# Kernel tuning notes

Measured on AMD Instinct MI355X. Metric: run time of the kernel, lower is better.

The kernel has to match this reference:

```python
import jax, jax.numpy as jnp
import numpy as np

P = 128; D = 128; A = 128
NS = D * A            # sinogram nodes
NP = P * P            # pixel nodes
N = NS + NP           # total graph nodes
EPS = 1e-5
_PNAMES = ["af_w1","af_b1","af_p1","af_bn_g","af_bn_b","af_w2","af_b2","af_p2","af_w3","af_b3","af_p3","af_w4","af_b4","af_p4","af_w5","af_b5","af_p5","gcn_w","gcn_b","sr_w1","sr_b1","sr_p1","sr_w2","sr_b2","sr_p2","sr_w3","sr_b3","sr_p3"]


def _conv(x, w, b, pad):
    y = jax.lax.conv_general_dilated(x, w, (1, 1), [(pad, pad), (pad, pad)],
                                     dimension_numbers=("NCHW", "OIHW", "NCHW"))
    return y + b[None, :, None, None]


def _prelu(x, a):
    return jnp.where(x >= 0, x, a * x)


def _bn(x, g, b):
    # BatchNorm2d in training mode: biased batch stats over (N,H,W)
    m = x.mean(axis=(0, 2, 3), keepdims=True)
    v = x.var(axis=(0, 2, 3), keepdims=True)
    return (x - m) * jax.lax.rsqrt(v + EPS) * g[None, :, None, None] + b[None, :, None, None]


def _forward(sino, edge_index, edge_weight, p):
    # AndrewCNN sinogram filter: 1 -> 64 -> 64 -> 64 -> 64 -> 8, 7x7 convs
    h = _prelu(_conv(sino, p["af_w1"], p["af_b1"], 3), p["af_p1"])
    h = _bn(h, p["af_bn_g"], p["af_bn_b"])
    h = _prelu(_conv(h, p["af_w2"], p["af_b2"], 3), p["af_p2"])
    h = _prelu(_conv(h, p["af_w3"], p["af_b3"], 3), p["af_p3"])
    h = _prelu(_conv(h, p["af_w4"], p["af_b4"], 3), p["af_p4"])
    h = _prelu(_conv(h, p["af_w5"], p["af_b5"], 3), p["af_p5"])   # [B,8,D,A]
    B, F = h.shape[0], h.shape[1]
    # build_nodes_features (source_to_target): sino nodes first, zero pixel nodes
    flat_sino = h.transpose(0, 2, 3, 1).reshape(B, NS, F)
    x = jnp.concatenate([flat_sino, jnp.zeros((B, NP, F), h.dtype)], axis=1)  # [B,N,8]
    # GCNConv(8,10): lin -> gcn_norm with self loops -> scatter-add at targets -> +bias
    xl = x @ p["gcn_w"]                                            # [B,N,10]
    row, col = edge_index[0], edge_index[1]
    loop = jnp.arange(N)
    row2 = jnp.concatenate([row, loop])
    col2 = jnp.concatenate([col, loop])
    w2 = jnp.concatenate([edge_weight, jnp.ones((N,), edge_weight.dtype)])
    deg = jnp.zeros((N,), xl.dtype).at[col2].add(w2)
    dis = jnp.where(deg > 0, jax.lax.rsqrt(jnp.maximum(deg, EPS * 0 + 1e-30)), 0.0)
    norm = dis[row2] * w2 * dis[col2]                              # [E+N]
    msgs = xl[:, row2, :] * norm[None, :, None]                    # [B,E+N,10]
    agg = jnp.zeros_like(xl).at[:, col2, :].add(msgs) + p["gcn_b"]
    # keep pixel nodes, reshape to image grid
    img = agg[:, NS:, :].transpose(0, 2, 1).reshape(B, -1, P, P)   # [B,10,P,P]
    # SRNET: 10 -> 64 (9x9) -> 32 (1x1) -> 1 (5x5)
    o = _prelu(_conv(img, p["sr_w1"], p["sr_b1"], 4), p["sr_p1"])
    o = _prelu(_conv(o,   p["sr_w2"], p["sr_b2"], 0), p["sr_p2"])
    o = _prelu(_conv(o,   p["sr_w3"], p["sr_b3"], 2), p["sr_p3"])
    return o


def setup_inputs() -> dict:
    f = jnp.float32
    ks = jax.random.split(jax.random.key(0), 16)
    B, E = 4, 2097152
    def rn(k, shape, s):
        return jax.random.normal(k, shape, f) * s
    inp = {
        "sino": jax.random.normal(ks[0], (B, 1, D, A), f),
        "edge_index": jax.random.randint(ks[1], (2, E), 0, N),
        "edge_weight": jax.random.uniform(ks[2], (E,), f),
    }
    kw = jax.random.split(ks[3], 9)
    inp["af_w1"] = rn(kw[0], (64, 1, 7, 7), 0.2)
    inp["af_w2"] = rn(kw[1], (64, 64, 7, 7), 0.03)
    inp["af_w3"] = rn(kw[2], (64, 64, 7, 7), 0.03)
    inp["af_w4"] = rn(kw[3], (64, 64, 7, 7), 0.03)
    inp["af_w5"] = rn(kw[4], (8, 64, 7, 7), 0.03)
    inp["gcn_w"] = rn(kw[5], (8, 10), 0.3)
    inp["sr_w1"] = rn(kw[6], (64, 10, 9, 9), 0.05)
    inp["sr_w2"] = rn(kw[7], (32, 64, 1, 1), 0.18)
    inp["sr_w3"] = rn(kw[8], (1, 32, 5, 5), 0.05)
    for nm, c in [("af_b1", 64), ("af_b2", 64), ("af_b3", 64), ("af_b4", 64), ("af_b5", 8), ("sr_b1", 64), ("sr_b2", 32), ("sr_b3", 1)]:
        inp[nm] = jnp.zeros((c,), f)
    inp["gcn_b"] = jnp.zeros((10,), f)
    inp["af_bn_g"] = jnp.ones((64,), f)
    inp["af_bn_b"] = jnp.zeros((64,), f)
    for nm in ["af_p1", "af_p2", "af_p3", "af_p4", "af_p5", "sr_p1", "sr_p2", "sr_p3"]:
        inp[nm] = jnp.array(0.25, f)
    return inp


def reference(sino, edge_index, edge_weight, af_w1, af_b1, af_p1, af_bn_g, af_bn_b, af_w2, af_b2, af_p2, af_w3, af_b3, af_p3, af_w4, af_b4, af_p4, af_w5, af_b5, af_p5, gcn_w, gcn_b, sr_w1, sr_b1, sr_p1, sr_w2, sr_b2, sr_p2, sr_w3, sr_b3, sr_p3):
    p = dict(zip(_PNAMES, (af_w1, af_b1, af_p1, af_bn_g, af_bn_b, af_w2, af_b2, af_p2, af_w3, af_b3, af_p3, af_w4, af_b4, af_p4, af_w5, af_b5, af_p5, gcn_w, gcn_b, sr_w1, sr_b1, sr_p1, sr_w2, sr_b2, sr_p2, sr_w3, sr_b3, sr_p3)))
    return _forward(sino, edge_index, edge_weight, p)
```

## Files before the change

kernel.cpp:

```cpp
#include <hip/hip_runtime.h>

static constexpr int NS = 16384;

typedef __attribute__((ext_vector_type(8))) short bf16x8;
typedef __attribute__((ext_vector_type(4))) float f32x4;

__device__ inline unsigned short bf16_rne(float x) {
  unsigned u = __float_as_uint(x);
  unsigned r = u + 0x7FFF + ((u >> 16) & 1);
  return (unsigned short)(r >> 16);
}

__global__ void k_wtrans(const float* __restrict__ w, float* __restrict__ wT,
                         int CO, int CI_IN, int CI_OUT, int KS) {
  int i = blockIdx.x * 256 + threadIdx.x;
  int tot = KS * KS * CI_OUT * CO;
  if (i >= tot) return;
  int co = i % CO;
  int r = i / CO;
  int ci = r % CI_OUT;
  int t = r / CI_OUT;
  int ky = t / KS, kx = t % KS;
  float v = 0.f;
  if (ci < CI_IN) v = w[((co * CI_IN + ci) * KS + ky) * KS + kx];
  wT[i] = v;
}

__global__ void k_wpack(const float* __restrict__ w, unsigned short* __restrict__ wpk) {
  int i = blockIdx.x * 256 + threadIdx.x;
  if (i >= 49 * 64 * 64) return;
  int co = i & 63, r = i >> 6;
  int ci = r & 63, tap = r >> 6;
  float v = w[(co * 64 + ci) * 49 + tap];
  unsigned short hi = bf16_rne(v);
  float hif = __uint_as_float((unsigned)hi << 16);
  unsigned short lo = bf16_rne(v - hif);
  int ks = ci >> 5, k32 = ci & 31;
  int lane = ((k32 >> 3) << 4) | (co & 15);
  int j = ci & 7, nt = co >> 4;
  size_t base = ((size_t)(((tap * 2 + ks) * 4 + nt) * 2) * 64 + lane) * 8 + j;
  wpk[base] = hi;
  wpk[base + 512] = lo;
}

__global__ void k_wpack5(const float* __restrict__ w5,
                         unsigned short* __restrict__ wpk) {
  int i = blockIdx.x * 256 + threadIdx.x;
  if (i >= 196 * 512) return;
  int j = i & 7, l = (i >> 3) & 63, f = i >> 9;
  int sp = f & 1, r = f >> 1;
  int ks = r & 1, tap = r >> 1;
  int co = l & 15;
  int k32 = ((l >> 4) << 3) + j;
  int ci = ks * 32 + k32;
  float v = (co < 8) ? w5[(co * 64 + ci) * 49 + tap] : 0.f;
  unsigned short hi = bf16_rne(v);
  unsigned short outv;
  if (sp == 0) {
    outv = hi;
  } else {
    float hif = __uint_as_float((unsigned)hi << 16);
    outv = bf16_rne(v - hif);
  }
  wpk[i] = outv;
}

__global__ void k_wpacks(const float* __restrict__ sw1,
                         unsigned short* __restrict__ wpk) {
  int i = blockIdx.x * 256 + threadIdx.x;
  if (i >= 360 * 512) return;
  int j = i & 7, l = (i >> 3) & 63, f = i >> 9;
  int sp = f & 1, nt = (f >> 1) & 3;
  int r3 = f >> 3, p = r3 % 5, ky = r3 / 5;
  int co = nt * 16 + (l & 15);
  int k = ((l >> 4) << 3) + j;
  int kx = 2 * p + (k >> 4);
  int ci = k & 15;
  float v = (ci < 10 && kx < 9) ? sw1[((co * 10 + ci) * 9 + ky) * 9 + kx] : 0.f;
  unsigned short hi = bf16_rne(v);
  unsigned short outv;
  if (sp == 0) {
    outv = hi;
  } else {
    float hif = __uint_as_float((unsigned)hi << 16);
    outv = bf16_rne(v - hif);
  }
  wpk[i] = outv;
}

__global__ __launch_bounds__(128) void k_conv1(
    const float* __restrict__ sino, const float* __restrict__ wT1,
    const float* __restrict__ b1, const float* __restrict__ p1,
    float* __restrict__ out) {
  int b = blockIdx.x >> 7, y = blockIdx.x & 127, x = threadIdx.x;
  float acc[64];
#pragma unroll
  for (int i = 0; i < 64; ++i) acc[i] = 0.f;
#pragma unroll
  for (int ky = 0; ky < 7; ++ky) {
    int yy = y + ky - 3;
#pragma unroll
    for (int kx = 0; kx < 7; ++kx) {
      int xx = x + kx - 3;
      float v = (yy >= 0 && yy < 128 && xx >= 0 && xx < 128)
                    ? sino[(b * 128 + yy) * 128 + xx]
                    : 0.f;
      const float* wr = wT1 + (ky * 7 + kx) * 64;
#pragma unroll
      for (int co = 0; co < 64; ++co) acc[co] += v * wr[co];
    }
  }
  float a = p1[0];
  float* op = out + ((size_t)(b * 134 + y + 3) * 134 + x + 3) * 64;
#pragma unroll
  for (int co = 0; co < 64; ++co) {
    float v = acc[co] + b1[co];
    op[co] = v >= 0.f ? v : a * v;
  }
}

__global__ __launch_bounds__(256) void k_bnstats(const float* __restrict__ x1p,
                                                 double* __restrict__ bnsum) {
  int c = threadIdx.x & 63, sl = threadIdx.x >> 6;
  double s = 0.0, q = 0.0;
  int base = blockIdx.x * 512 + sl * 128;
  for (int i = 0; i < 128; ++i) {
    int p = base + i;
    int b = p >> 14, y = (p >> 7) & 127, x = p & 127;
    double v = (double)x1p[((size_t)(b * 134 + y + 3) * 134 + x + 3) * 64 + c];
    s += v;
    q += v * v;
  }
  __shared__ double red[2][4][64];
  red[0][sl][c] = s;
  red[1][sl][c] = q;
  __syncthreads();
  if (sl == 0) {
    s = red[0][0][c] + red[0][1][c] + red[0][2][c] + red[0][3][c];
    q = red[1][0][c] + red[1][1][c] + red[1][2][c] + red[1][3][c];
    atomicAdd(&bnsum[c], s);
    atomicAdd(&bnsum[64 + c], q);
  }
}

__global__ void k_bnfinal(const double* __restrict__ bnsum, float* __restrict__ bnsc,
                          const float* __restrict__ g, const float* __restrict__ bb) {
  int c = threadIdx.x;
  if (c >= 64) return;
  double m = bnsum[c] * (1.0 / 65536.0);
  double v = bnsum[64 + c] * (1.0 / 65536.0) - m * m;
  double sc = (double)g[c] * rsqrt(v + 1e-5);
  bnsc[c] = (float)sc;
  bnsc[64 + c] = (float)((double)bb[c] - m * sc);
}

__global__ __launch_bounds__(256) void k_bnapply(
    const float* __restrict__ x1p, const float* __restrict__ bnsc,
    unsigned short* __restrict__ oh, unsigned short* __restrict__ ol) {
  int i = blockIdx.x * 256 + threadIdx.x;
  if (i >= 4 * 128 * 128 * 16) return;
  int g = i & 15, p = i >> 4;
  int b = p >> 14, y = (p >> 7) & 127, x = p & 127;
  size_t base = ((size_t)(b * 134 + y + 3) * 134 + x + 3) * 64 + g * 4;
  float4 v = *(const float4*)(x1p + base);
  int c = g * 4;
  v.x = v.x * bnsc[c + 0] + bnsc[64 + c + 0];
  v.y = v.y * bnsc[c + 1] + bnsc[64 + c + 1];
  v.z = v.z * bnsc[c + 2] + bnsc[64 + c + 2];
  v.w = v.w * bnsc[c + 3] + bnsc[64 + c + 3];
  unsigned short h0 = bf16_rne(v.x), h1 = bf16_rne(v.y);
  unsigned short h2 = bf16_rne(v.z), h3 = bf16_rne(v.w);
  unsigned short l0 = bf16_rne(v.x - __uint_as_float((unsigned)h0 << 16));
  unsigned short l1 = bf16_rne(v.y - __uint_as_float((unsigned)h1 << 16));
  unsigned short l2 = bf16_rne(v.z - __uint_as_float((unsigned)h2 << 16));
  unsigned short l3 = bf16_rne(v.w - __uint_as_float((unsigned)h3 << 16));
  *(ushort4*)(oh + base) = make_ushort4(h0, h1, h2, h3);
  *(ushort4*)(ol + base) = make_ushort4(l0, l1, l2, l3);
}

__global__ __launch_bounds__(256) void k_convm(
    const unsigned short* __restrict__ inh, const unsigned short* __restrict__ inl,
    const unsigned short* __restrict__ wpk, const float* __restrict__ bias,
    const float* __restrict__ alpha, unsigned short* __restrict__ outh,
    unsigned short* __restrict__ outl) {
  int i0 = (int)((blockIdx.x & 7) * 64 + (blockIdx.x >> 3));
  int b = i0 >> 7, y = i0 & 127;
  int tid = threadIdx.x, l = tid & 63;
  int wv = tid >> 6;
  int pxb = (wv & 1) * 64;
  int coh = wv >> 1;
  int lg = l >> 4, lm = l & 15;

  __shared__ unsigned short hbuf[2][134 * 44];
  __shared__ unsigned short lbuf[2][134 * 44];

  f32x4 acc[4][2];
#pragma unroll
  for (int mt = 0; mt < 4; ++mt)
#pragma unroll
    for (int ntl = 0; ntl < 2; ++ntl) acc[mt][ntl] = (f32x4){0.f, 0.f, 0.f, 0.f};

  for (int ch = 0; ch < 64; ch += 32) {
    auto stage = [&](int ky, int s) {
      const unsigned short* gh = inh + ((size_t)(b * 134 + y + ky) * 134) * 64 + ch;
      const unsigned short* gl = inl + ((size_t)(b * 134 + y + ky) * 134) * 64 + ch;
      for (int i = tid; i < 134 * 4; i += 256) {
        int px = i >> 2, q = i & 3;
        bf16x8 vh = *(const bf16x8*)(gh + px * 64 + q * 8);
        bf16x8 vl = *(const bf16x8*)(gl + px * 64 + q * 8);
        *(bf16x8*)&hbuf[s][px * 44 + q * 8] = vh;
        *(bf16x8*)&lbuf[s][px * 44 + q * 8] = vl;
      }
    };
    stage(0, 0);
    __syncthreads();
    for (int ky = 0; ky < 7; ++ky) {
      if (ky < 6) stage(ky + 1, (ky + 1) & 1);
      int s = ky & 1;
#pragma unroll
      for (int kx = 0; kx < 7; ++kx) {
        int tap = ky * 7 + kx;
        const unsigned short* wt =
            wpk + (size_t)(tap * 2 + (ch >> 5)) * 8 * 512 + (size_t)l * 8;
        bf16x8 Bh[2], Bl[2];
#pragma unroll
        for (int ntl = 0; ntl < 2; ++ntl) {
          int nt = coh * 2 + ntl;
          Bh[ntl] = *(const bf16x8*)(wt + (nt * 2 + 0) * 512);
          Bl[ntl] = *(const bf16x8*)(wt + (nt * 2 + 1) * 512);
        }
#pragma unroll
        for (int mt = 0; mt < 4; ++mt) {
          int px = pxb + mt * 16 + lm + kx;
          bf16x8 Ah = *(const bf16x8*)&hbuf[s][px * 44 + lg * 8];
          bf16x8 Al = *(const bf16x8*)&lbuf[s][px * 44 + lg * 8];
#pragma unroll
          for (int ntl = 0; ntl < 2; ++ntl) {
            acc[mt][ntl] = __builtin_amdgcn_mfma_f32_16x16x32_bf16(Ah, Bh[ntl],
                                                                   acc[mt][ntl], 0, 0, 0);
            acc[mt][ntl] = __builtin_amdgcn_mfma_f32_16x16x32_bf16(Ah, Bl[ntl],
                                                                   acc[mt][ntl], 0, 0, 0);
            acc[mt][ntl] = __builtin_amdgcn_mfma_f32_16x16x32_bf16(Al, Bh[ntl],
                                                                   acc[mt][ntl], 0, 0, 0);
          }
        }
      }
      __syncthreads();
    }
  }
  float a = alpha[0];
#pragma unroll
  for (int mt = 0; mt < 4; ++mt)
#pragma unroll
    for (int ntl = 0; ntl < 2; ++ntl)
#pragma unroll
      for (int r = 0; r < 4; ++r) {
        int px = pxb + mt * 16 + lg * 4 + r;
        int co = coh * 32 + ntl * 16 + lm;
        float v = acc[mt][ntl][r] + bias[co];
        v = v >= 0.f ? v : a * v;
        unsigned short h = bf16_rne(v);
        unsigned short lo = bf16_rne(v - __uint_as_float((unsigned)h << 16));
        size_t idx = ((size_t)(b * 134 + y + 3) * 134 + px + 3) * 64 + co;
        outh[idx] = h;
        outl[idx] = lo;
      }
}

__global__ __launch_bounds__(256) void k_convm5(
    const unsigned short* __restrict__ inh, const unsigned short* __restrict__ inl,
    const unsigned short* __restrict__ wpk, const float* __restrict__ b5,
    const float* __restrict__ p5, const float* __restrict__ gw,
    float* __restrict__ xl) {
  int i0 = (int)((blockIdx.x & 7) * 64 + (blockIdx.x >> 3));
  int b = i0 >> 7, y = i0 & 127;
  int tid = threadIdx.x, l = tid & 63;
  int wv = tid >> 6;
  int pxb = wv * 32;
  int lg = l >> 4, lm = l & 15;

  __shared__ unsigned short hbuf[2][134 * 44];
  __shared__ unsigned short lbuf[2][134 * 44];
  __shared__ float feat[128][9];

  f32x4 acc[2];
  acc[0] = (f32x4){0.f, 0.f, 0.f, 0.f};
  acc[1] = (f32x4){0.f, 0.f, 0.f, 0.f};

  for (int ch = 0; ch < 64; ch += 32) {
    auto stage = [&](int ky, int s) {
      const unsigned short* gh = inh + ((size_t)(b * 134 + y + ky) * 134) * 64 + ch;
      const unsigned short* gl = inl + ((size_t)(b * 134 + y + ky) * 134) * 64 + ch;
      for (int i = tid; i < 134 * 4; i += 256) {
        int px = i >> 2, q = i & 3;
        bf16x8 vh = *(const bf16x8*)(gh + px * 64 + q * 8);
        bf16x8 vl = *(const bf16x8*)(gl + px * 64 + q * 8);
        *(bf16x8*)&hbuf[s][px * 44 + q * 8] = vh;
        *(bf16x8*)&lbuf[s][px * 44 + q * 8] = vl;
      }
    };
    stage(0, 0);
    __syncthreads();
    for (int ky = 0; ky < 7; ++ky) {
      if (ky < 6) stage(ky + 1, (ky + 1) & 1);
      int s = ky & 1;
#pragma unroll
      for (int kx = 0; kx < 7; ++kx) {
        int tap = ky * 7 + kx;
        const unsigned short* wt =
            wpk + (size_t)((tap * 2 + (ch >> 5)) * 2) * 512 + (size_t)l * 8;
        bf16x8 Bh = *(const bf16x8*)(wt);
        bf16x8 Bl = *(const bf16x8*)(wt + 512);
#pragma unroll
        for (int mt = 0; mt < 2; ++mt) {
          int px = pxb + mt * 16 + lm + kx;
          bf16x8 Ah = *(const bf16x8*)&hbuf[s][px * 44 + lg * 8];
          bf16x8 Al = *(const bf16x8*)&lbuf[s][px * 44 + lg * 8];
          acc[mt] = __builtin_amdgcn_mfma_f32_16x16x32_bf16(Ah, Bh, acc[mt], 0, 0, 0);
          acc[mt] = __builtin_amdgcn_mfma_f32_16x16x32_bf16(Ah, Bl, acc[mt], 0, 0, 0);
          acc[mt] = __builtin_amdgcn_mfma_f32_16x16x32_bf16(Al, Bh, acc[mt], 0, 0, 0);
        }
      }
      __syncthreads();
    }
  }
  float a = p5[0];
  if (lm < 8) {
#pragma unroll
    for (int mt = 0; mt < 2; ++mt)
#pragma unroll
      for (int r = 0; r < 4; ++r) {
        int px = pxb + mt * 16 + lg * 4 + r;
        float v = acc[mt][r] + b5[lm];
        feat[px][lm] = v >= 0.f ? v : a * v;
      }
  }
  __syncthreads();
  if (tid < 128) {
    int px = tid;
    float o[10];
#pragma unroll
    for (int f = 0; f < 10; ++f) o[f] = 0.f;
#pragma unroll
    for (int c = 0; c < 8; ++c) {
      float fv = feat[px][c];
#pragma unroll
      for (int f = 0; f < 10; ++f) o[f] += fv * gw[c * 10 + f];
    }
    float* op = xl + ((size_t)b * 16384 + y * 128 + px) * 10;
#pragma unroll
    for (int f = 0; f < 10; ++f) op[f] = o[f];
  }
}

__global__ __launch_bounds__(256) void k_convs(
    const float* __restrict__ imgp, const unsigned short* __restrict__ wpk,
    const float* __restrict__ bias, const float* __restrict__ alpha,
    float* __restrict__ out) {
  int i0 = (int)((blockIdx.x & 7) * 64 + (blockIdx.x >> 3));
  int b = i0 >> 7, y = i0 & 127;
  int tid = threadIdx.x, l = tid & 63;
  int wv = tid >> 6, wbase = wv * 32;
  int lg = l >> 4, lm = l & 15;

  __shared__ unsigned short hbuf[2][137 * 20];
  __shared__ unsigned short lbuf[2][137 * 20];

  f32x4 acc[2][4];
#pragma unroll
  for (int mt = 0; mt < 2; ++mt)
#pragma unroll
    for (int nt = 0; nt < 4; ++nt) acc[mt][nt] = (f32x4){0.f, 0.f, 0.f, 0.f};

  auto stage = [&](int ky, int s) {
    const float* gin = imgp + ((size_t)(b * 136 + y + ky) * 136) * 16;
    for (int i = tid; i < 137 * 4; i += 256) {
      int px = i >> 2, q = i & 3;
      float4 v = (px < 136) ? *(const float4*)(gin + px * 16 + q * 4)
                            : make_float4(0.f, 0.f, 0.f, 0.f);
      unsigned short h0 = bf16_rne(v.x), h1 = bf16_rne(v.y);
      unsigned short h2 = bf16_rne(v.z), h3 = bf16_rne(v.w);
      unsigned short l0 = bf16_rne(v.x - __uint_as_float((unsigned)h0 << 16));
      unsigned short l1 = bf16_rne(v.y - __uint_as_float((unsigned)h1 << 16));
      unsigned short l2 = bf16_rne(v.z - __uint_as_float((unsigned)h2 << 16));
      unsigned short l3 = bf16_rne(v.w - __uint_as_float((unsigned)h3 << 16));
      *(ushort4*)&hbuf[s][px * 20 + q * 4] = make_ushort4(h0, h1, h2, h3);
      *(ushort4*)&lbuf[s][px * 20 + q * 4] = make_ushort4(l0, l1, l2, l3);
    }
  };
  stage(0, 0);
  __syncthreads();
  for (int ky = 0; ky < 9; ++ky) {
    if (ky < 8) stage(ky + 1, (ky + 1) & 1);
    int s = ky & 1;
#pragma unroll
    for (int p = 0; p < 5; ++p) {
      const unsigned short* wt =
          wpk + ((size_t)(ky * 5 + p) * 8) * 512 + (size_t)l * 8;
      bf16x8 Bh[4], Bl[4];
#pragma unroll
      for (int nt = 0; nt < 4; ++nt) {
        Bh[nt] = *(const bf16x8*)(wt + (nt * 2 + 0) * 512);
        Bl[nt] = *(const bf16x8*)(wt + (nt * 2 + 1) * 512);
      }
#pragma unroll
      for (int mt = 0; mt < 2; ++mt) {
        int px = wbase + mt * 16 + lm + 2 * p + (lg >> 1);
        bf16x8 Ah = *(const bf16x8*)&hbuf[s][px * 20 + (lg & 1) * 8];
        bf16x8 Al = *(const bf16x8*)&lbuf[s][px * 20 + (lg & 1) * 8];
#pragma unroll
        for (int nt = 0; nt < 4; ++nt) {
          acc[mt][nt] =
              __builtin_amdgcn_mfma_f32_16x16x32_bf16(Ah, Bh[nt], acc[mt][nt], 0, 0, 0);
          acc[mt][nt] =
              __builtin_amdgcn_mfma_f32_16x16x32_bf16(Ah, Bl[nt], acc[mt][nt], 0, 0, 0);
          acc[mt][nt] =
              __builtin_amdgcn_mfma_f32_16x16x32_bf16(Al, Bh[nt], acc[mt][nt], 0, 0, 0);
        }
      }
    }
    __syncthreads();
  }
  float a = alpha[0];
#pragma unroll
  for (int mt = 0; mt < 2; ++mt)
#pragma unroll
    for (int nt = 0; nt < 4; ++nt)
#pragma unroll
      for (int r = 0; r < 4; ++r) {
        int px = wbase + mt * 16 + lg * 4 + r;
        int co = nt * 16 + lm;
        float v = acc[mt][nt][r] + bias[co];
        out[((size_t)(b * 128 + y) * 128 + px) * 64 + co] = v >= 0.f ? v : a * v;
      }
}

template <int CIN, int COUT, int KS, int IN_H, int IN_W, int OUT_H, int OUT_W,
          int OUT_OFF, int STR, int CH, int NSPLIT>
__global__ __launch_bounds__(64 * NSPLIT) void k_conv3(
    const float* __restrict__ in, const float* __restrict__ wT,
    const float* __restrict__ bias, const float* __restrict__ alpha,
    float* __restrict__ out) {
  constexpr int C = COUT / NSPLIT;
  int b = blockIdx.x >> 6, y0 = (blockIdx.x & 63) * 2;
  int l = threadIdx.x & 63;
  int cob = __builtin_amdgcn_readfirstlane((int)(threadIdx.x >> 6) * C);
  __shared__ float sbuf[2][IN_W * STR];
  float acc[4][C];
#pragma unroll
  for (int r = 0; r < 4; ++r)
#pragma unroll
    for (int i = 0; i < C; ++i) acc[r][i] = 0.f;

  for (int ch = 0; ch < CIN; ch += CH) {
    auto stage = [&](int k) {
      const float* gin = in + ((size_t)(b * IN_H + y0 + k) * IN_W) * CIN + ch;
      float* dst = sbuf[k & 1];
      constexpr int N4 = IN_W * CH / 4;
      for (int i = threadIdx.x; i < N4; i += 64 * NSPLIT) {
        int xx = i / (CH / 4), c4 = (i - xx * (CH / 4)) * 4;
        float4 v = *(const float4*)(gin + (size_t)xx * CIN + c4);
        *(float4*)(dst + xx * STR + c4) = v;
      }
    };
    stage(0);
    stage(1);
    __syncthreads();
    for (int ky = 0; ky < KS; ++ky) {
      const float* sA = sbuf[ky & 1];
      const float* sB = sbuf[(ky + 1) & 1];
      for (int kx = 0; kx < KS; ++kx) {
        const float* wt = wT + ((size_t)(ky * KS + kx) * CIN + ch) * COUT + cob;
        const float* a0p = sA + (l + kx) * STR;
        const float* a1p = sA + (l + 64 + kx) * STR;
        const float* b0p = sB + (l + kx) * STR;
        const float* b1p = sB + (l + 64 + kx) * STR;
#pragma unroll
        for (int ci = 0; ci < CH; ci += 4) {
          float4 a0 = *(const float4*)(a0p + ci);
          float4 a1 = *(const float4*)(a1p + ci);
          float4 b0 = *(const float4*)(b0p + ci);
          float4 b1 = *(const float4*)(b1p + ci);
#pragma unroll
          for (int c = 0; c < 4; ++c) {
            const float* wr = wt + (size_t)(ci + c) * COUT;
            float va0 = ((const float*)&a0)[c], va1 = ((const float*)&a1)[c];
            float vb0 = ((const float*)&b0)[c], vb1 = ((const float*)&b1)[c];
#pragma unroll
            for (int co = 0; co < C; ++co) {
              float w = wr[co];
              acc[0][co] += va0 * w;
              acc[1][co] += va1 * w;
              acc[2][co] += vb0 * w;
              acc[3][co] += vb1 * w;
            }
          }
        }
      }
      __syncthreads();
      if (ky < KS - 1) {
        stage(ky + 2);
        __syncthreads();
      }
    }
  }
  float a = alpha[0];
#pragma unroll
  for (int r = 0; r < 2; ++r) {
    float* rowp =
        out + (((size_t)(b * OUT_H + y0 + r + OUT_OFF)) * OUT_W + OUT_OFF) * COUT + cob;
#pragma unroll
    for (int p = 0; p < 2; ++p) {
      float* op = rowp + (size_t)(l + p * 64) * COUT;
#pragma unroll
      for (int co = 0; co < C; ++co) {
        float v = acc[r * 2 + p][co] + bias[cob + co];
        op[co] = v >= 0.f ? v : a * v;
      }
    }
  }
}

template <int CIN, int COUT, int KS, int IN_H, int IN_W, int OUT_H, int OUT_W,
          int OUT_OFF, int STR, int NSPLIT>
__global__ __launch_bounds__(64 * NSPLIT) void k_conv2(
    const float* __restrict__ in, const float* __restrict__ wT,
    const float* __restrict__ bias, const float* __restrict__ alpha,
    float* __restrict__ out) {
  constexpr int C = COUT / NSPLIT;
  int b = blockIdx.x >> 7, y = blockIdx.x & 127;
  int l = threadIdx.x & 63;
  int cob = __builtin_amdgcn_readfirstlane((int)(threadIdx.x >> 6) * C);
  __shared__ float srow[IN_W * STR];
  float acc0[C], acc1[C];
#pragma unroll
  for (int i = 0; i < C; ++i) acc0[i] = acc1[i] = 0.f;

  for (int ky = 0; ky < KS; ++ky) {
    __syncthreads();
    const float* gin = in + (size_t)(b * IN_H + y + ky) * IN_W * CIN;
    constexpr int N4 = IN_W * CIN / 4;
    for (int i = threadIdx.x; i < N4; i += 64 * NSPLIT) {
      float4 v = *(const float4*)(gin + (size_t)i * 4);
      int xx = (i * 4) / CIN, cc = (i * 4) % CIN;
      *(float4*)(srow + xx * STR + cc) = v;
    }
    __syncthreads();
    for (int kx = 0; kx < KS; ++kx) {
      const float* wt = wT + ((size_t)(ky * KS + kx) * CIN) * COUT + cob;
      const float* s0 = srow + (l + kx) * STR;
      const float* s1 = srow + (l + 64 + kx) * STR;
      for (int ci = 0; ci < CIN; ci += 4) {
        float4 a0 = *(const float4*)(s0 + ci);
        float4 a1 = *(const float4*)(s1 + ci);
#pragma unroll
        for (int c = 0; c < 4; ++c) {
          float v0 = ((const float*)&a0)[c];
          float v1 = ((const float*)&a1)[c];
          const float* wr = wt + (size_t)(ci + c) * COUT;
#pragma unroll
          for (int co = 0; co < C; ++co) {
            float w = wr[co];
            acc0[co] += v0 * w;
            acc1[co] += v1 * w;
          }
        }
      }
    }
  }
  float a = alpha[0];
  float* rowp = out + ((size_t)(b * OUT_H + y + OUT_OFF) * OUT_W + OUT_OFF) * COUT + cob;
  float* op0 = rowp + (size_t)l * COUT;
  float* op1 = rowp + (size_t)(l + 64) * COUT;
#pragma unroll
  for (int co = 0; co < C; ++co) {
    float bi = bias[cob + co];
    float v0 = acc0[co] + bi;
    float v1 = acc1[co] + bi;
    op0[co] = v0 >= 0.f ? v0 : a * v0;
    op1[co] = v1 >= 0.f ? v1 : a * v1;
  }
}

template <int HALF>
__global__ __launch_bounds__(1024) void k_degp(
    const int* __restrict__ ei, const float* __restrict__ ew,
    float* __restrict__ pdeg, int* __restrict__ cnt, int* __restrict__ rank, int E) {
  __shared__ float degl[16384];
  for (int i = threadIdx.x; i < 16384; i += 1024) degl[i] = 0.f;
  __syncthreads();
  int chunk = (E + gridDim.x - 1) / gridDim.x;
  int base = blockIdx.x * chunk;
  int end = min(E, base + chunk);
  for (int e = base + (int)threadIdx.x; e < end; e += 1024) {
    int col = ei[E + e];
    float w = ew[e];
    if ((col >> 14) == HALF) atomicAdd(&degl[col & 16383], w);
    if (HALF == 1) {
      int row = ei[e];
      if (row < NS && col >= NS) rank[e] = atomicAdd(&cnt[col - NS], 1);
    }
  }
  __syncthreads();
  float* pd = pdeg + (size_t)blockIdx.x * 16384;
  for (int i = threadIdx.x; i < 16384; i += 1024) pd[i] = degl[i];
}

__global__ void k_dis2(const float* __restrict__ pdegA, const float* __restrict__ pdegB,
                       float* __restrict__ dis, int nb) {
  int n = blockIdx.x * 256 + threadIdx.x;
  if (n >= 2 * NS) return;
  const float* p = (n < NS ? pdegA : pdegB) + (n & 16383);
  float s = 1.0f;
  for (int b = 0; b < nb; ++b) s += p[(size_t)b * 16384];
  dis[n] = rsqrtf(s);
}

__global__ __launch_bounds__(1024) void k_scan(const int* __restrict__ cnt,
                                               int* __restrict__ ptr) {
  __shared__ int ps[1024];
  int tid = threadIdx.x;
  int base = tid * 16;
  int v[16];
  int s = 0;
#pragma unroll
  for (int k = 0; k < 16; ++k) {
    v[k] = s;
    s += cnt[base + k];
  }
  ps[tid] = s;
  __syncthreads();
  for (int off = 1; off < 1024; off <<= 1) {
    int t = (tid >= off) ? ps[tid - off] : 0;
    __syncthreads();
    ps[tid] += t;
    __syncthreads();
  }
  int chunkoff = (tid == 0) ? 0 : ps[tid - 1];
#pragma unroll
  for (int k = 0; k < 16; ++k) ptr[base + k] = chunkoff + v[k];
  if (tid == 1023) ptr[16384] = ps[1023];
}

__global__ void k_bucket2(const int* __restrict__ ei, const float* __restrict__ ew,
                          const float* __restrict__ dis, const int* __restrict__ ptr,
                          const int* __restrict__ rank, int* __restrict__ erow,
                          float* __restrict__ enrm, int E) {
  int e = blockIdx.x * 256 + threadIdx.x;
  if (e >= E) return;
  int row = ei[e], col = ei[E + e];
  if (row >= NS || col < NS) return;
  int cp = col - NS;
  int pos = ptr[cp] + rank[e];
  erow[pos] = row;
  enrm[pos] = dis[row] * ew[e] * dis[col];
}

__global__ __launch_bounds__(256) void k_gather(
    const int* __restrict__ ptr, const int* __restrict__ erow,
    const float* __restrict__ enrm, const float* __restrict__ xl,
    const float* __restrict__ gb, float* __restrict__ imgp) {
  int cp = blockIdx.x * 4 + (threadIdx.x >> 6);
  int l = threadIdx.x & 63;
  int b = l >> 4, f = l & 15;
  bool act = f < 10;
  float acc = 0.f;
  int s = ptr[cp], e1 = ptr[cp + 1];
  for (int e = s; e < e1; ++e) {
    int row = erow[e];
    float nrm = enrm[e];
    if (act) acc += xl[((size_t)b * 16384 + row) * 10 + f] * nrm;
  }
  if (act) {
    int y = cp >> 7, x = cp & 127;
    imgp[((size_t)(b * 136 + y + 4) * 136 + x + 4) * 16 + f] = acc + gb[f];
  }
}

extern "C" void kernel_launch(void* const* d_in, const int* in_sizes, int n_in,
                              void* d_out, int out_size, void* d_ws, size_t ws_size,
                              hipStream_t stream) {
  const float* sino = (const float*)d_in[0];
  const int* ei = (const int*)d_in[1];
  const float* ew = (const float*)d_in[2];
  const float* w1 = (const float*)d_in[3];
  const float* w2 = (const float*)d_in[4];
  const float* w3 = (const float*)d_in[5];
  const float* w4 = (const float*)d_in[6];
  const float* w5 = (const float*)d_in[7];
  const float* gw = (const float*)d_in[8];
  const float* sw1 = (const float*)d_in[9];
  const float* sw2 = (const float*)d_in[10];
  const float* sw3 = (const float*)d_in[11];
  const float* b1 = (const float*)d_in[12];
  const float* b2 = (const float*)d_in[13];
  const float* b3 = (const float*)d_in[14];
  const float* b4 = (const float*)d_in[15];
  const float* b5 = (const float*)d_in[16];
  const float* sb1 = (const float*)d_in[17];
  const float* sb2 = (const float*)d_in[18];
  const float* sb3 = (const float*)d_in[19];
  const float* gb = (const float*)d_in[20];
  const float* bng = (const float*)d_in[21];
  const float* bnb = (const float*)d_in[22];
  const float* p1 = (const float*)d_in[23];
  const float* p2 = (const float*)d_in[24];
  const float* p3 = (const float*)d_in[25];
  const float* p4 = (const float*)d_in[26];
  const float* p5 = (const float*)d_in[27];
  const float* sp1 = (const float*)d_in[28];
  const float* sp2 = (const float*)d_in[29];
  const float* sp3 = (const float*)d_in[30];
  const int E = in_sizes[2];

  char* ws = (char*)d_ws;
  size_t off = 0;
  auto alloc = [&](size_t bytes) {
    char* p = ws + off;
    off += (bytes + 255) & ~(size_t)255;
    return p;
  };
  const size_t PL = (size_t)4 * 134 * 134 * 64;
  float* x1p = (float*)alloc(PL * 4);
  unsigned short* xh1 = (unsigned short*)alloc(PL * 2);
  unsigned short* xl1 = (unsigned short*)alloc(PL * 2);
  unsigned short* xh2 = (unsigned short*)alloc(PL * 2);
  unsigned short* xl2 = (unsigned short*)alloc(PL * 2);
  unsigned short* wpk2 = (unsigned short*)alloc(401408 * 2);
  unsigned short* wpk3 = (unsigned short*)alloc(401408 * 2);
  unsigned short* wpk4 = (unsigned short*)alloc(401408 * 2);
  unsigned short* wpk5 = (unsigned short*)alloc(100352 * 2);
  unsigned short* wpks1 = (unsigned short*)alloc(184320 * 2);
  float* wt1 = (float*)alloc(3136 * 4);
  float* wts2 = (float*)alloc(2048 * 4);
  float* wts3 = (float*)alloc(800 * 4);
  double* bnsum = (double*)alloc(128 * 8);
  float* bnsc = (float*)alloc(128 * 4);
  float* xl = (float*)alloc((size_t)4 * 16384 * 10 * 4);
  float* pdegA = (float*)alloc((size_t)128 * 16384 * 4);
  float* pdegB = (float*)alloc((size_t)128 * 16384 * 4);
  float* dis = (float*)alloc(32768 * 4);
  int* cnt = (int*)alloc(16384 * 4);
  int* ptr = (int*)alloc(16385 * 4);
  int* rank = (int*)alloc((size_t)E * 4);
  int* erow = (int*)alloc((size_t)E * 4);
  float* enrm = (float*)alloc((size_t)E * 4);
  float* imgp = (float*)alloc((size_t)4 * 136 * 136 * 16 * 4);
  float* s1 = (float*)alloc((size_t)4 * 128 * 128 * 64 * 4);
  float* s2p = (float*)alloc((size_t)4 * 132 * 132 * 32 * 4);

  hipMemsetAsync(xh1, 0, PL * 2, stream);
  hipMemsetAsync(xl1, 0, PL * 2, stream);
  hipMemsetAsync(xh2, 0, PL * 2, stream);
  hipMemsetAsync(xl2, 0, PL * 2, stream);
  hipMemsetAsync(bnsum, 0, 128 * 8, stream);
  hipMemsetAsync(cnt, 0, 16384 * 4, stream);
  hipMemsetAsync(imgp, 0, (size_t)4 * 136 * 136 * 16 * 4, stream);
  hipMemsetAsync(s2p, 0, (size_t)4 * 132 * 132 * 32 * 4, stream);

  k_wpack<<<784, 256, 0, stream>>>(w2, wpk2);
  k_wpack<<<784, 256, 0, stream>>>(w3, wpk3);
  k_wpack<<<784, 256, 0, stream>>>(w4, wpk4);
  k_wpack5<<<392, 256, 0, stream>>>(w5, wpk5);
  k_wpacks<<<720, 256, 0, stream>>>(sw1, wpks1);
  k_wtrans<<<13, 256, 0, stream>>>(w1, wt1, 64, 1, 1, 7);
  k_wtrans<<<8, 256, 0, stream>>>(sw2, wts2, 32, 64, 64, 1);
  k_wtrans<<<4, 256, 0, stream>>>(sw3, wts3, 1, 32, 32, 5);

  k_conv1<<<512, 128, 0, stream>>>(sino, wt1, b1, p1, x1p);
  k_bnstats<<<128, 256, 0, stream>>>(x1p, bnsum);
  k_bnfinal<<<1, 64, 0, stream>>>(bnsum, bnsc, bng, bnb);
  k_bnapply<<<4096, 256, 0, stream>>>(x1p, bnsc, xh1, xl1);

  k_convm<<<512, 256, 0, stream>>>(xh1, xl1, wpk2, b2, p2, xh2, xl2);
  k_convm<<<512, 256, 0, stream>>>(xh2, xl2, wpk3, b3, p3, xh1, xl1);
  k_convm<<<512, 256, 0, stream>>>(xh1, xl1, wpk4, b4, p4, xh2, xl2);
  k_convm5<<<512, 256, 0, stream>>>(xh2, xl2, wpk5, b5, p5, gw, xl);

  k_degp<0><<<128, 1024, 0, stream>>>(ei, ew, pdegA, cnt, rank, E);
  k_degp<1><<<128, 1024, 0, stream>>>(ei, ew, pdegB, cnt, rank, E);
  k_dis2<<<128, 256, 0, stream>>>(pdegA, pdegB, dis, 128);
  k_scan<<<1, 1024, 0, stream>>>(cnt, ptr);
  k_bucket2<<<(E + 255) / 256, 256, 0, stream>>>(ei, ew, dis, ptr, rank, erow, enrm, E);
  k_gather<<<4096, 256, 0, stream>>>(ptr, erow, enrm, xl, gb, imgp);

  k_convs<<<512, 256, 0, stream>>>(imgp, wpks1, sb1, sp1, s1);
  k_conv3<64, 32, 1, 128, 128, 132, 132, 2, 36, 32, 8>
      <<<256, 512, 0, stream>>>(s1, wts2, sb2, sp2, s2p);
  k_conv2<32, 1, 5, 132, 132, 128, 128, 0, 36, 1>
      <<<512, 64, 0, stream>>>(s2p, wts3, sb3, sp3, (float*)d_out);
}
```

Before: 630.0 us.

## Compute two output rows per block in 7x7 MFMA convs to share staged input rows

```diff
diff --git a/kernel.cpp b/kernel.cpp
--- a/kernel.cpp
+++ b/kernel.cpp
@@ -178,17 +178,18 @@
   *(ushort4*)(ol + base) = make_ushort4(l0, l1, l2, l3);
 }
 
-__global__ __launch_bounds__(256) void k_convm(
+__global__ __launch_bounds__(512) void k_convm(
     const unsigned short* __restrict__ inh, const unsigned short* __restrict__ inl,
     const unsigned short* __restrict__ wpk, const float* __restrict__ bias,
     const float* __restrict__ alpha, unsigned short* __restrict__ outh,
     unsigned short* __restrict__ outl) {
-  int i0 = (int)((blockIdx.x & 7) * 64 + (blockIdx.x >> 3));
-  int b = i0 >> 7, y = i0 & 127;
+  int i0 = (int)((blockIdx.x & 7) * 32 + (blockIdx.x >> 3));
+  int b = i0 >> 6, y0 = (i0 & 63) * 2;
   int tid = threadIdx.x, l = tid & 63;
   int wv = tid >> 6;
-  int pxb = (wv & 1) * 64;
-  int coh = wv >> 1;
+  int row = wv >> 2;
+  int pxb = ((wv >> 1) & 1) * 64;
+  int coh = wv & 1;
   int lg = l >> 4, lm = l & 15;
 
   __shared__ unsigned short hbuf[2][134 * 44];
@@ -201,22 +202,26 @@
     for (int ntl = 0; ntl < 2; ++ntl) acc[mt][ntl] = (f32x4){0.f, 0.f, 0.f, 0.f};
 
   for (int ch = 0; ch < 64; ch += 32) {
-    auto stage = [&](int ky, int s) {
-      const unsigned short* gh = inh + ((size_t)(b * 134 + y + ky) * 134) * 64 + ch;
-      const unsigned short* gl = inl + ((size_t)(b * 134 + y + ky) * 134) * 64 + ch;
-      for (int i = tid; i < 134 * 4; i += 256) {
+    auto stage = [&](int k) {
+      const unsigned short* gh = inh + ((size_t)(b * 134 + y0 + k) * 134) * 64 + ch;
+      const unsigned short* gl = inl + ((size_t)(b * 134 + y0 + k) * 134) * 64 + ch;
+      unsigned short* dh = hbuf[k & 1];
+      unsigned short* dl = lbuf[k & 1];
+      for (int i = tid; i < 134 * 4; i += 512) {
         int px = i >> 2, q = i & 3;
         bf16x8 vh = *(const bf16x8*)(gh + px * 64 + q * 8);
         bf16x8 vl = *(const bf16x8*)(gl + px * 64 + q * 8);
-        *(bf16x8*)&hbuf[s][px * 44 + q * 8] = vh;
-        *(bf16x8*)&lbuf[s][px * 44 + q * 8] = vl;
+        *(bf16x8*)&dh[px * 44 + q * 8] = vh;
+        *(bf16x8*)&dl[px * 44 + q * 8] = vl;
       }
     };
-    stage(0, 0);
+    stage(0);
+    stage(1);
     __syncthreads();
     for (int ky = 0; ky < 7; ++ky) {
-      if (ky < 6) stage(ky + 1, (ky + 1) & 1);
-      int s = ky & 1;
+      int s = (ky + row) & 1;
+      const unsigned short* hb = hbuf[s];
+      const unsigned short* lb = lbuf[s];
 #pragma unroll
       for (int kx = 0; kx < 7; ++kx) {
         int tap = ky * 7 + kx;
@@ -232,8 +237,8 @@
 #pragma unroll
         for (int mt = 0; mt < 4; ++mt) {
           int px = pxb + mt * 16 + lm + kx;
-          bf16x8 Ah = *(const bf16x8*)&hbuf[s][px * 44 + lg * 8];
-          bf16x8 Al = *(const bf16x8*)&lbuf[s][px * 44 + lg * 8];
+          bf16x8 Ah = *(const bf16x8*)&hb[px * 44 + lg * 8];
+          bf16x8 Al = *(const bf16x8*)&lb[px * 44 + lg * 8];
 #pragma unroll
           for (int ntl = 0; ntl < 2; ++ntl) {
             acc[mt][ntl] = __builtin_amdgcn_mfma_f32_16x16x32_bf16(Ah, Bh[ntl],
@@ -246,6 +251,10 @@
         }
       }
       __syncthreads();
+      if (ky < 6) {
+        stage(ky + 2);
+        __syncthreads();
+      }
     }
   }
   float a = alpha[0];
@@ -261,49 +270,54 @@
         v = v >= 0.f ? v : a * v;
         unsigned short h = bf16_rne(v);
         unsigned short lo = bf16_rne(v - __uint_as_float((unsigned)h << 16));
-        size_t idx = ((size_t)(b * 134 + y + 3) * 134 + px + 3) * 64 + co;
+        size_t idx = ((size_t)(b * 134 + y0 + row + 3) * 134 + px + 3) * 64 + co;
         outh[idx] = h;
         outl[idx] = lo;
       }
 }
 
-__global__ __launch_bounds__(256) void k_convm5(
+__global__ __launch_bounds__(512) void k_convm5(
     const unsigned short* __restrict__ inh, const unsigned short* __restrict__ inl,
     const unsigned short* __restrict__ wpk, const float* __restrict__ b5,
     const float* __restrict__ p5, const float* __restrict__ gw,
     float* __restrict__ xl) {
-  int i0 = (int)((blockIdx.x & 7) * 64 + (blockIdx.x >> 3));
-  int b = i0 >> 7, y = i0 & 127;
+  int i0 = (int)((blockIdx.x & 7) * 32 + (blockIdx.x >> 3));
+  int b = i0 >> 6, y0 = (i0 & 63) * 2;
   int tid = threadIdx.x, l = tid & 63;
   int wv = tid >> 6;
-  int pxb = wv * 32;
+  int row = wv >> 2;
+  int pxb = (wv & 3) * 32;
   int lg = l >> 4, lm = l & 15;
 
   __shared__ unsigned short hbuf[2][134 * 44];
   __shared__ unsigned short lbuf[2][134 * 44];
-  __shared__ float feat[128][9];
+  __shared__ float feat[2][128][9];
 
   f32x4 acc[2];
   acc[0] = (f32x4){0.f, 0.f, 0.f, 0.f};
   acc[1] = (f32x4){0.f, 0.f, 0.f, 0.f};
 
   for (int ch = 0; ch < 64; ch += 32) {
-    auto stage = [&](int ky, int s) {
-      const unsigned short* gh = inh + ((size_t)(b * 134 + y + ky) * 134) * 64 + ch;
-      const unsigned short* gl = inl + ((size_t)(b * 134 + y + ky) * 134) * 64 + ch;
-      for (int i = tid; i < 134 * 4; i += 256) {
+    auto stage = [&](int k) {
+      const unsigned short* gh = inh + ((size_t)(b * 134 + y0 + k) * 134) * 64 + ch;
+      const unsigned short* gl = inl + ((size_t)(b * 134 + y0 + k) * 134) * 64 + ch;
+      unsigned short* dh = hbuf[k & 1];
+      unsigned short* dl = lbuf[k & 1];
+      for (int i = tid; i < 134 * 4; i += 512) {
         int px = i >> 2, q = i & 3;
         bf16x8 vh = *(const bf16x8*)(gh + px * 64 + q * 8);
         bf16x8 vl = *(const bf16x8*)(gl + px * 64 + q * 8);
-        *(bf16x8*)&hbuf[s][px * 44 + q * 8] = vh;
-        *(bf16x8*)&lbuf[s][px * 44 + q * 8] = vl;
+        *(bf16x8*)&dh[px * 44 + q * 8] = vh;
+        *(bf16x8*)&dl[px * 44 + q * 8] = vl;
       }
     };
-    stage(0, 0);
+    stage(0);
+    stage(1);
     __syncthreads();
     for (int ky = 0; ky < 7; ++ky) {
-      if (ky < 6) stage(ky + 1, (ky + 1) & 1);
-      int s = ky & 1;
+      int s = (ky + row) & 1;
+      const unsigned short* hb = hbuf[s];
+      const unsigned short* lb = lbuf[s];
 #pragma unroll
       for (int kx = 0; kx < 7; ++kx) {
         int tap = ky * 7 + kx;
@@ -314,14 +328,18 @@
 #pragma unroll
         for (int mt = 0; mt < 2; ++mt) {
           int px = pxb + mt * 16 + lm + kx;
-          bf16x8 Ah = *(const bf16x8*)&hbuf[s][px * 44 + lg * 8];
-          bf16x8 Al = *(const bf16x8*)&lbuf[s][px * 44 + lg * 8];
+          bf16x8 Ah = *(const bf16x8*)&hb[px * 44 + lg * 8];
+          bf16x8 Al = *(const bf16x8*)&lb[px * 44 + lg * 8];
           acc[mt] = __builtin_amdgcn_mfma_f32_16x16x32_bf16(Ah, Bh, acc[mt], 0, 0, 0);
           acc[mt] = __builtin_amdgcn_mfma_f32_16x16x32_bf16(Ah, Bl, acc[mt], 0, 0, 0);
           acc[mt] = __builtin_amdgcn_mfma_f32_16x16x32_bf16(Al, Bh, acc[mt], 0, 0, 0);
         }
       }
       __syncthreads();
+      if (ky < 6) {
+        stage(ky + 2);
+        __syncthreads();
+      }
     }
   }
   float a = p5[0];
@@ -332,22 +350,22 @@
       for (int r = 0; r < 4; ++r) {
         int px = pxb + mt * 16 + lg * 4 + r;
         float v = acc[mt][r] + b5[lm];
-        feat[px][lm] = v >= 0.f ? v : a * v;
+        feat[row][px][lm] = v >= 0.f ? v : a * v;
       }
   }
   __syncthreads();
-  if (tid < 128) {
-    int px = tid;
+  if (tid < 256) {
+    int rr = tid >> 7, px = tid & 127;
     float o[10];
 #pragma unroll
     for (int f = 0; f < 10; ++f) o[f] = 0.f;
 #pragma unroll
     for (int c = 0; c < 8; ++c) {
-      float fv = feat[px][c];
+      float fv = feat[rr][px][c];
 #pragma unroll
       for (int f = 0; f < 10; ++f) o[f] += fv * gw[c * 10 + f];
     }
-    float* op = xl + ((size_t)b * 16384 + y * 128 + px) * 10;
+    float* op = xl + ((size_t)b * 16384 + (y0 + rr) * 128 + px) * 10;
 #pragma unroll
     for (int f = 0; f < 10; ++f) op[f] = o[f];
   }
@@ -772,10 +790,10 @@
   k_bnfinal<<<1, 64, 0, stream>>>(bnsum, bnsc, bng, bnb);
   k_bnapply<<<4096, 256, 0, stream>>>(x1p, bnsc, xh1, xl1);
 
-  k_convm<<<512, 256, 0, stream>>>(xh1, xl1, wpk2, b2, p2, xh2, xl2);
-  k_convm<<<512, 256, 0, stream>>>(xh2, xl2, wpk3, b3, p3, xh1, xl1);
-  k_convm<<<512, 256, 0, stream>>>(xh1, xl1, wpk4, b4, p4, xh2, xl2);
-  k_convm5<<<512, 256, 0, stream>>>(xh2, xl2, wpk5, b5, p5, gw, xl);
+  k_convm<<<256, 512, 0, stream>>>(xh1, xl1, wpk2, b2, p2, xh2, xl2);
+  k_convm<<<256, 512, 0, stream>>>(xh2, xl2, wpk3, b3, p3, xh1, xl1);
+  k_convm<<<256, 512, 0, stream>>>(xh1, xl1, wpk4, b4, p4, xh2, xl2);
+  k_convm5<<<256, 512, 0, stream>>>(xh2, xl2, wpk5, b5, p5, gw, xl);
 
   k_degp<0><<<128, 1024, 0, stream>>>(ei, ew, pdegA, cnt, rank, E);
   k_degp<1><<<128, 1024, 0, stream>>>(ei, ew, pdegB, cnt, rank, E);
```

Measured after the change: 1.055 ms. 1.67x slower.
